# Performance work log

Hardware: AMD Instinct MI355X
Metric: run time of the kernel (lower is better)

Reference implementation:

```python
import jax, jax.numpy as jnp
import numpy as np

B, T, C = 4, 2048, 1024
N_HEADS = 16
HEAD_DIM = C // N_HEADS


def rotary_embedding(seq_len, dim, dtype=jnp.float32):
    pos = jnp.arange(seq_len, dtype=dtype)[:, None]
    i = jnp.arange(0, dim, 2, dtype=dtype)[None, :]
    theta = pos / jnp.power(10000.0, i / dim)
    return jnp.cos(theta), jnp.sin(theta)


def apply_rotary(x, cos, sin):
    # x: [B, T, H, D]; cos/sin: [T, D//2]
    d = x.shape[-1]
    x1, x2 = x[..., : d // 2], x[..., d // 2 :]
    rotated = jnp.concatenate([-x2, x1], axis=-1)
    cos = jnp.concatenate([cos, cos], axis=-1)[None, :, None, :]
    sin = jnp.concatenate([sin, sin], axis=-1)[None, :, None, :]
    return x * cos + rotated * sin


def setup_inputs() -> dict:
    key = jax.random.key(0)
    k1, k2, k3 = jax.random.split(key, 3)
    x = jax.random.normal(k1, (B, T, C), dtype=jnp.float32)
    # lecun_normal-ish init scale
    w_qkv = jax.random.normal(k2, (C, 3 * C), dtype=jnp.float32) / np.sqrt(C)
    w_out = jax.random.normal(k3, (C, C), dtype=jnp.float32) / np.sqrt(C)
    return {"x": x, "w_qkv": w_qkv, "w_out": w_out}


def reference(x, w_qkv, w_out):
    b, t, c = x.shape
    qkv = jnp.einsum("btc,cd->btd", x, w_qkv)
    q, k, v = jnp.split(qkv, 3, axis=-1)
    q = q.reshape(b, t, N_HEADS, HEAD_DIM)
    k = k.reshape(b, t, N_HEADS, HEAD_DIM)
    v = v.reshape(b, t, N_HEADS, HEAD_DIM)
    cos, sin = rotary_embedding(t, HEAD_DIM, dtype=x.dtype)
    q = apply_rotary(q, cos, sin)
    k = apply_rotary(k, cos, sin)
    scale = jnp.sqrt(jnp.asarray(HEAD_DIM, dtype=x.dtype))
    # scores: [B, H, T, T]
    attn = jnp.einsum("bqhd,bkhd->bhqk", q, k) / scale
    mask = jnp.tril(jnp.ones((t, t), dtype=jnp.bool_))
    attn = jnp.where(mask[None, None, :, :], attn, jnp.asarray(-1e9, dtype=x.dtype))
    attn = jax.nn.softmax(attn, axis=-1)
    out = jnp.einsum("bhqk,bkhd->bqhd", attn, v).reshape(b, t, c)
    return jnp.einsum("btc,cd->btd", out, w_out)
```

## Files before the change

kernel.cpp:

```cpp
#include <hip/hip_runtime.h>
#include <stdint.h>

#define DEVI __device__ __forceinline__

typedef unsigned short ushort_t;
typedef __bf16 bf16x8 __attribute__((ext_vector_type(8)));
typedef float f32x4 __attribute__((ext_vector_type(4)));
typedef unsigned short ushort8 __attribute__((ext_vector_type(8)));
typedef short s16x4 __attribute__((ext_vector_type(4)));

#define BB 4
#define TT 2048
#define CC 1024
#define NH 16
#define HD 64
#define MM (BB*TT)

DEVI ushort_t f2bf(float f) {
    union { float f; unsigned u; } v; v.f = f;
    return (ushort_t)((v.u + 0x7FFFu + ((v.u >> 16) & 1u)) >> 16);
}

typedef const __attribute__((address_space(1))) unsigned int guint_t;
typedef __attribute__((address_space(3))) unsigned int luint_t;

DEVI void gl2lds16(const void* g, void* lds) {
    __builtin_amdgcn_global_load_lds((guint_t*)(uintptr_t)g,
                                     (luint_t*)(unsigned int)(uintptr_t)lds,
                                     16, 0, 0);
}

__global__ void cvt_f32_bf16(const float* __restrict__ in,
                             ushort_t* __restrict__ out) {
    int i = blockIdx.x * 256 + threadIdx.x;
    const float4* p = (const float4*)in + (size_t)i * 2;
    float4 a = p[0], b = p[1];
    ushort8 r;
    r[0] = f2bf(a.x); r[1] = f2bf(a.y); r[2] = f2bf(a.z); r[3] = f2bf(a.w);
    r[4] = f2bf(b.x); r[5] = f2bf(b.y); r[6] = f2bf(b.z); r[7] = f2bf(b.w);
    *(ushort8*)(out + (size_t)i * 8) = r;
}

__global__ void transpose_f2b(const float* __restrict__ in,
                              ushort_t* __restrict__ out, int R, int Cc) {
    __shared__ ushort_t tile[32][33];
    int bx = blockIdx.x * 32;
    int by = blockIdx.y * 32;
    int tx = threadIdx.x & 31, ty = threadIdx.x >> 5;
    #pragma unroll
    for (int i = 0; i < 4; i++) {
        int r = ty * 4 + i;
        tile[r][tx] = f2bf(in[(size_t)(by + r) * Cc + bx + tx]);
    }
    __syncthreads();
    #pragma unroll
    for (int i = 0; i < 4; i++) {
        int r = ty * 4 + i;
        out[(size_t)(bx + r) * R + by + tx] = tile[tx][r];
    }
}

__global__ void rope_table(float2* __restrict__ tab) {
    int i = blockIdx.x * 256 + threadIdx.x;
    int t = i >> 5, j = i & 31;
    float inv = exp2f((float)j * -0.41524101186092029f);
    float theta = (float)t * inv;
    float s, c;
    sincosf(theta, &s, &c);
    tab[i] = make_float2(c, s);
}

__global__ void vtrans(const ushort_t* __restrict__ Vb,
                       ushort_t* __restrict__ VbT) {
    __shared__ ushort_t tile[64 * 72];
    const int bh = blockIdx.y;
    const int t0 = blockIdx.x * 64;
    const int tid = threadIdx.x;
    const int r = tid >> 2, c = (tid & 3) * 16;
    const size_t base = (size_t)bh * (TT * HD);
    const ushort_t* g = Vb + base + (size_t)(t0 + r) * HD + c;
    *(ushort8*)&tile[r * 72 + c]     = *(const ushort8*)g;
    *(ushort8*)&tile[r * 72 + c + 8] = *(const ushort8*)(g + 8);
    __syncthreads();
    ushort8 a, b;
    #pragma unroll
    for (int j = 0; j < 8; j++) a[j] = tile[(c + j) * 72 + r];
    #pragma unroll
    for (int j = 0; j < 8; j++) b[j] = tile[(c + 8 + j) * 72 + r];
    ushort_t* o = VbT + base + (size_t)r * TT + t0 + c;
    *(ushort8*)o = a;
    *(ushort8*)(o + 8) = b;
}

template <int MODE>
__global__ __launch_bounds__(256, 2) void gemm_bt(
    const ushort_t* __restrict__ A, const ushort_t* __restrict__ Bt,
    float* __restrict__ CoutF,
    ushort_t* __restrict__ Qb, ushort_t* __restrict__ Kb, ushort_t* __restrict__ Vb,
    const float2* __restrict__ rope, int M, int N, int Kd) {
    __shared__ __attribute__((aligned(16))) ushort_t As[128 * 32];
    __shared__ __attribute__((aligned(16))) ushort_t Bs[128 * 32];

    const int tid = threadIdx.x;
    const int w = tid >> 6, l = tid & 63;
    const int lane15 = l & 15, quad = l >> 4;
    const int wm = (w >> 1) * 64, wn = (w & 1) * 64;
    const int bm = blockIdx.y, bn = blockIdx.x;

    f32x4 acc[4][4];
    #pragma unroll
    for (int i = 0; i < 4; i++)
        #pragma unroll
        for (int j = 0; j < 4; j++)
            acc[i][j] = f32x4{0.f, 0.f, 0.f, 0.f};

    const int c0 = w * 2, c1 = w * 2 + 1;
    const int lr = l >> 2, lc = (l & 3) * 8;
    const int rowA0 = bm * 128 + c0 * 16 + lr;
    const int rowA1 = bm * 128 + c1 * 16 + lr;
    const ushort_t *gA0, *gA1;
    if (MODE == 2) {
        gA0 = A + ((size_t)(rowA0 >> 11) * 32768 + (rowA0 & (TT - 1))) * HD + lc;
        gA1 = A + ((size_t)(rowA1 >> 11) * 32768 + (rowA1 & (TT - 1))) * HD + lc;
    } else {
        gA0 = A + (size_t)rowA0 * Kd + lc;
        gA1 = A + (size_t)rowA1 * Kd + lc;
    }
    const ushort_t* gB0 = Bt + (size_t)(bn * 128 + c0 * 16 + lr) * Kd + lc;
    const ushort_t* gB1 = Bt + (size_t)(bn * 128 + c1 * 16 + lr) * Kd + lc;

    for (int k0 = 0; k0 < Kd; k0 += 32) {
        size_t offA = (MODE == 2) ? ((size_t)(k0 >> 6) * 131072 + (size_t)(k0 & 63))
                                  : (size_t)k0;
        __syncthreads();
        gl2lds16(gA0 + offA, &As[c0 * 512]);
        gl2lds16(gA1 + offA, &As[c1 * 512]);
        gl2lds16(gB0 + k0,  &Bs[c0 * 512]);
        gl2lds16(gB1 + k0,  &Bs[c1 * 512]);
        __syncthreads();

        bf16x8 af[4], bf[4];
        #pragma unroll
        for (int t = 0; t < 4; t++) {
            af[t] = *(const bf16x8*)&As[(wm + t * 16 + lane15) * 32 + quad * 8];
            bf[t] = *(const bf16x8*)&Bs[(wn + t * 16 + lane15) * 32 + quad * 8];
        }
        #pragma unroll
        for (int tm = 0; tm < 4; tm++)
            #pragma unroll
            for (int tn = 0; tn < 4; tn++)
                acc[tm][tn] = __builtin_amdgcn_mfma_f32_16x16x32_bf16(
                    af[tm], bf[tn], acc[tm][tn], 0, 0, 0);
    }

    if (MODE == 2) {
        #pragma unroll
        for (int tm = 0; tm < 4; tm++) {
            int row0 = bm * 128 + wm + tm * 16 + quad * 4;
            #pragma unroll
            for (int r = 0; r < 4; r++) {
                size_t rb = (size_t)(row0 + r) * N + bn * 128 + wn;
                #pragma unroll
                for (int tn = 0; tn < 4; tn++)
                    CoutF[rb + tn * 16 + lane15] = acc[tm][tn][r];
            }
        }
    } else {
        const float SCQ = 0.125f * 1.4426950408889634f;
        const int colbase = bn * 128 + wn;
        const int seg = colbase >> 10;
        const int h = (colbase & 1023) >> 6;
        #pragma unroll
        for (int tm = 0; tm < 4; tm++) {
            int row0 = bm * 128 + wm + tm * 16 + quad * 4;
            #pragma unroll
            for (int r = 0; r < 4; r++) {
                int row = row0 + r;
                int b = row >> 11, t = row & (TT - 1);
                size_t ob = ((size_t)(b * NH + h) * TT + t) * HD;
                if (seg == 2) {
                    #pragma unroll
                    for (int tn = 0; tn < 4; tn++)
                        Vb[ob + tn * 16 + lane15] = f2bf(acc[tm][tn][r]);
                } else {
                    ushort_t* dst = (seg == 0) ? Qb : Kb;
                    #pragma unroll
                    for (int tn = 0; tn < 2; tn++) {
                        int j = tn * 16 + lane15;
                        float2 cs = rope[t * 32 + j];
                        float x1 = acc[tm][tn][r];
                        float x2 = acc[tm][tn + 2][r];
                        float y1 = x1 * cs.x - x2 * cs.y;
                        float y2 = x2 * cs.x + x1 * cs.y;
                        if (seg == 0) { y1 *= SCQ; y2 *= SCQ; }
                        dst[ob + j]      = f2bf(y1);
                        dst[ob + 32 + j] = f2bf(y2);
                    }
                }
            }
        }
    }
}

__global__ __launch_bounds__(512, 4) void attn_kernel(
    ushort_t* __restrict__ Qb, const ushort_t* __restrict__ Kb,
    const ushort_t* __restrict__ VbT) {
    __shared__ __attribute__((aligned(16))) ushort_t Ks[64 * 72];
    __shared__ __attribute__((aligned(16))) ushort_t Vs[64 * 72];

    const int tid = threadIdx.x;
    const int w = tid >> 6, l = tid & 63;
    const int lane15 = l & 15, quad = l >> 4;
    const int bh = blockIdx.y;
    const size_t base = (size_t)bh * (TT * HD);

    const int sr = tid >> 3;
    const int sd = (tid & 7) * 8;
    const ushort_t* kgb = Kb  + base + (size_t)sr * HD + sd;
    const ushort_t* vgb = VbT + base + (size_t)sr * TT + sd;

    #pragma unroll
    for (int seg = 0; seg < 2; seg++) {
        const int qt = (seg == 0) ? (int)blockIdx.x : (15 - (int)blockIdx.x);
        const int q0 = qt * 128;
        const int rbase = q0 + w * 16;
        const int ktmax = 2 * qt + 1;

        bf16x8 qf0, qf1;
        {
            const ushort_t* qp = Qb + base + (size_t)(rbase + lane15) * HD + quad * 8;
            qf0 = *(const bf16x8*)qp;
            qf1 = *(const bf16x8*)(qp + 32);
        }

        f32x4 o[4];
        #pragma unroll
        for (int nt = 0; nt < 4; nt++) o[nt] = f32x4{0.f, 0.f, 0.f, 0.f};
        float mrow = -INFINITY, lrow = 0.f;

        ushort8 kr = *(const ushort8*)kgb;
        ushort8 vr = *(const ushort8*)vgb;

        for (int kt = 0; kt <= ktmax; kt++) {
            __syncthreads();
            *(ushort8*)&Ks[sr * 72 + sd] = kr;
            *(ushort8*)&Vs[sr * 72 + sd] = vr;
            __syncthreads();
            if (kt < ktmax) {
                kr = *(const ushort8*)(kgb + (size_t)(kt + 1) * 64 * HD);
                vr = *(const ushort8*)(vgb + (size_t)(kt + 1) * 64);
            }

            f32x4 s[4];
            #pragma unroll
            for (int c = 0; c < 4; c++) {
                bf16x8 k0 = *(const bf16x8*)&Ks[(c * 16 + lane15) * 72 + quad * 8];
                bf16x8 k1 = *(const bf16x8*)&Ks[(c * 16 + lane15) * 72 + 32 + quad * 8];
                f32x4 z = f32x4{0.f, 0.f, 0.f, 0.f};
                z = __builtin_amdgcn_mfma_f32_16x16x32_bf16(k0, qf0, z, 0, 0, 0);
                s[c] = __builtin_amdgcn_mfma_f32_16x16x32_bf16(k1, qf1, z, 0, 0, 0);
            }

            const int qrow = rbase + lane15;
            if (kt * 64 + 63 > rbase) {
                #pragma unroll
                for (int c = 0; c < 4; c++)
                    #pragma unroll
                    for (int r = 0; r < 4; r++)
                        if (kt * 64 + c * 16 + quad * 4 + r > qrow) s[c][r] = -1e9f;
            }

            float mt = s[0][0];
            #pragma unroll
            for (int c = 0; c < 4; c++)
                #pragma unroll
                for (int r = 0; r < 4; r++) mt = fmaxf(mt, s[c][r]);
            mt = fmaxf(mt, __shfl_xor(mt, 16, 64));
            mt = fmaxf(mt, __shfl_xor(mt, 32, 64));

            float mn = fmaxf(mrow, mt);
            float alpha = __builtin_amdgcn_exp2f(mrow - mn);
            mrow = mn;

            #pragma unroll
            for (int c = 0; c < 4; c++)
                #pragma unroll
                for (int r = 0; r < 4; r++)
                    s[c][r] = __builtin_amdgcn_exp2f(s[c][r] - mn);

            float rs = 0.f;
            #pragma unroll
            for (int c = 0; c < 4; c++)
                rs += (s[c][0] + s[c][1]) + (s[c][2] + s[c][3]);
            rs += __shfl_xor(rs, 16, 64);
            rs += __shfl_xor(rs, 32, 64);
            lrow = lrow * alpha + rs;

            #pragma unroll
            for (int r = 0; r < 4; r++) {
                float aO = __shfl(alpha, quad * 4 + r, 64);
                #pragma unroll
                for (int nt = 0; nt < 4; nt++) o[nt][r] *= aO;
            }

            #pragma unroll
            for (int c = 0; c < 4; c++) {
                s16x4 pf;
                #pragma unroll
                for (int r = 0; r < 4; r++) pf[r] = (short)f2bf(s[c][r]);
                #pragma unroll
                for (int nt = 0; nt < 4; nt++) {
                    s16x4 vf = *(const s16x4*)&Vs[(nt * 16 + lane15) * 72 +
                                                  c * 16 + quad * 4];
                    o[nt] = __builtin_amdgcn_mfma_f32_16x16x16bf16_1k(
                        pf, vf, o[nt], 0, 0, 0);
                }
            }
        }

        float linv = 1.0f / lrow;
        #pragma unroll
        for (int r = 0; r < 4; r++) {
            float lO = __shfl(linv, quad * 4 + r, 64);
            size_t rb = base + (size_t)(rbase + quad * 4 + r) * HD;
            #pragma unroll
            for (int nt = 0; nt < 4; nt++)
                Qb[rb + nt * 16 + lane15] = f2bf(o[nt][r] * lO);
        }
    }
}

extern "C" void kernel_launch(void* const* d_in, const int* in_sizes, int n_in,
                              void* d_out, int out_size, void* d_ws, size_t ws_size,
                              hipStream_t stream) {
    const float* x    = (const float*)d_in[0];
    const float* wqkv = (const float*)d_in[1];
    const float* wout = (const float*)d_in[2];
    float* out = (float*)d_out;

    char* ws = (char*)d_ws;
    ushort_t* WqkvT = (ushort_t*)(ws);
    ushort_t* WoutT = (ushort_t*)(ws + 6291456);
    float2*   rope  = (float2*)  (ws + 8388608);
    ushort_t* Xb    = (ushort_t*)(ws + 8912896);
    ushort_t* Qb    = (ushort_t*)(ws + 8912896 + 16777216);
    ushort_t* Kb    = (ushort_t*)(ws + 8912896 + 2 * 16777216);
    ushort_t* Vb    = (ushort_t*)(ws + 8912896 + 3 * 16777216);
    ushort_t* VbT   = Xb;

    cvt_f32_bf16<<<dim3(MM * CC / (256 * 8)), 256, 0, stream>>>(x, Xb);
    transpose_f2b<<<dim3(3 * CC / 32, CC / 32), 256, 0, stream>>>(wqkv, WqkvT, CC, 3 * CC);
    transpose_f2b<<<dim3(CC / 32, CC / 32), 256, 0, stream>>>(wout, WoutT, CC, CC);
    rope_table<<<dim3(256), 256, 0, stream>>>(rope);

    gemm_bt<1><<<dim3(3 * CC / 128, MM / 128), 256, 0, stream>>>(
        Xb, WqkvT, nullptr, Qb, Kb, Vb, rope, MM, 3 * CC, CC);

    vtrans<<<dim3(TT / 64, BB * NH), 256, 0, stream>>>(Vb, VbT);

    attn_kernel<<<dim3(8, BB * NH), 512, 0, stream>>>(Qb, Kb, VbT);

    gemm_bt<2><<<dim3(CC / 128, MM / 128), 256, 0, stream>>>(
        Qb, WoutT, out, nullptr, nullptr, nullptr, nullptr, MM, CC, CC);
}
```

Before: 279.3 us.

## Widen attention key tile to 128 and pack P to bf16 via perm truncation

```diff
diff --git a/kernel.cpp b/kernel.cpp
--- a/kernel.cpp
+++ b/kernel.cpp
@@ -8,6 +8,7 @@
 typedef float f32x4 __attribute__((ext_vector_type(4)));
 typedef unsigned short ushort8 __attribute__((ext_vector_type(8)));
 typedef short s16x4 __attribute__((ext_vector_type(4)));
+typedef unsigned int u32x2 __attribute__((ext_vector_type(2)));
 
 #define BB 4
 #define TT 2048
@@ -19,6 +20,11 @@
 DEVI ushort_t f2bf(float f) {
     union { float f; unsigned u; } v; v.f = f;
     return (ushort_t)((v.u + 0x7FFFu + ((v.u >> 16) & 1u)) >> 16);
+}
+
+DEVI unsigned pk_bf16(float lo, float hi) {
+    union { float f; unsigned u; } a, b; a.f = lo; b.f = hi;
+    return __builtin_amdgcn_perm(b.u, a.u, 0x07060302u);
 }
 
 typedef const __attribute__((address_space(1))) unsigned int guint_t;
@@ -202,29 +208,32 @@
     }
 }
 
+#define KS 72
+#define VS 136
 __global__ __launch_bounds__(512, 4) void attn_kernel(
     ushort_t* __restrict__ Qb, const ushort_t* __restrict__ Kb,
     const ushort_t* __restrict__ VbT) {
-    __shared__ __attribute__((aligned(16))) ushort_t Ks[64 * 72];
-    __shared__ __attribute__((aligned(16))) ushort_t Vs[64 * 72];
+    __shared__ __attribute__((aligned(16))) ushort_t Ks[128 * KS];
+    __shared__ __attribute__((aligned(16))) ushort_t Vs[64 * VS];
 
     const int tid = threadIdx.x;
-    const int w = tid >> 6, l = tid & 63;
+    const int l = tid & 63;
+    const int w = tid >> 6;
     const int lane15 = l & 15, quad = l >> 4;
     const int bh = blockIdx.y;
     const size_t base = (size_t)bh * (TT * HD);
 
-    const int sr = tid >> 3;
-    const int sd = (tid & 7) * 8;
-    const ushort_t* kgb = Kb  + base + (size_t)sr * HD + sd;
-    const ushort_t* vgb = VbT + base + (size_t)sr * TT + sd;
+    const int ksr = tid >> 3, ksd = (tid & 7) * 8;
+    const int vsr = tid >> 4, vsd = (tid & 15) * 8;
+    const ushort_t* kgb = Kb  + base + (size_t)ksr * HD + ksd;
+    const ushort_t* vgb = VbT + base + (size_t)vsr * TT + vsd;
 
     #pragma unroll
     for (int seg = 0; seg < 2; seg++) {
         const int qt = (seg == 0) ? (int)blockIdx.x : (15 - (int)blockIdx.x);
         const int q0 = qt * 128;
         const int rbase = q0 + w * 16;
-        const int ktmax = 2 * qt + 1;
+        const int ktmax = qt;
 
         bf16x8 qf0, qf1;
         {
@@ -238,43 +247,51 @@
         for (int nt = 0; nt < 4; nt++) o[nt] = f32x4{0.f, 0.f, 0.f, 0.f};
         float mrow = -INFINITY, lrow = 0.f;
 
-        ushort8 kr = *(const ushort8*)kgb;
-        ushort8 vr = *(const ushort8*)vgb;
+        ushort8 kr0 = *(const ushort8*)kgb;
+        ushort8 kr1 = *(const ushort8*)(kgb + (size_t)64 * HD);
+        ushort8 vr0 = *(const ushort8*)vgb;
+        ushort8 vr1 = *(const ushort8*)(vgb + (size_t)32 * TT);
 
         for (int kt = 0; kt <= ktmax; kt++) {
             __syncthreads();
-            *(ushort8*)&Ks[sr * 72 + sd] = kr;
-            *(ushort8*)&Vs[sr * 72 + sd] = vr;
+            *(ushort8*)&Ks[ksr * KS + ksd]        = kr0;
+            *(ushort8*)&Ks[(ksr + 64) * KS + ksd] = kr1;
+            *(ushort8*)&Vs[vsr * VS + vsd]        = vr0;
+            *(ushort8*)&Vs[(vsr + 32) * VS + vsd] = vr1;
             __syncthreads();
             if (kt < ktmax) {
-                kr = *(const ushort8*)(kgb + (size_t)(kt + 1) * 64 * HD);
-                vr = *(const ushort8*)(vgb + (size_t)(kt + 1) * 64);
-            }
-
-            f32x4 s[4];
-            #pragma unroll
-            for (int c = 0; c < 4; c++) {
-                bf16x8 k0 = *(const bf16x8*)&Ks[(c * 16 + lane15) * 72 + quad * 8];
-                bf16x8 k1 = *(const bf16x8*)&Ks[(c * 16 + lane15) * 72 + 32 + quad * 8];
+                const ushort_t* kg2 = kgb + (size_t)(kt + 1) * 128 * HD;
+                const ushort_t* vg2 = vgb + (size_t)(kt + 1) * 128;
+                kr0 = *(const ushort8*)kg2;
+                kr1 = *(const ushort8*)(kg2 + (size_t)64 * HD);
+                vr0 = *(const ushort8*)vg2;
+                vr1 = *(const ushort8*)(vg2 + (size_t)32 * TT);
+            }
+
+            f32x4 s[8];
+            #pragma unroll
+            for (int c = 0; c < 8; c++) {
+                bf16x8 k0 = *(const bf16x8*)&Ks[(c * 16 + lane15) * KS + quad * 8];
+                bf16x8 k1 = *(const bf16x8*)&Ks[(c * 16 + lane15) * KS + 32 + quad * 8];
                 f32x4 z = f32x4{0.f, 0.f, 0.f, 0.f};
                 z = __builtin_amdgcn_mfma_f32_16x16x32_bf16(k0, qf0, z, 0, 0, 0);
                 s[c] = __builtin_amdgcn_mfma_f32_16x16x32_bf16(k1, qf1, z, 0, 0, 0);
             }
 
             const int qrow = rbase + lane15;
-            if (kt * 64 + 63 > rbase) {
-                #pragma unroll
-                for (int c = 0; c < 4; c++)
+            if (kt == ktmax) {
+                #pragma unroll
+                for (int c = 0; c < 8; c++)
                     #pragma unroll
                     for (int r = 0; r < 4; r++)
-                        if (kt * 64 + c * 16 + quad * 4 + r > qrow) s[c][r] = -1e9f;
-            }
-
-            float mt = s[0][0];
-            #pragma unroll
-            for (int c = 0; c < 4; c++)
-                #pragma unroll
-                for (int r = 0; r < 4; r++) mt = fmaxf(mt, s[c][r]);
+                        if (kt * 128 + c * 16 + quad * 4 + r > qrow) s[c][r] = -1e9f;
+            }
+
+            float mt = fmaxf(fmaxf(fmaxf(s[0][0], s[0][1]), fmaxf(s[0][2], s[0][3])),
+                             fmaxf(fmaxf(s[1][0], s[1][1]), fmaxf(s[1][2], s[1][3])));
+            #pragma unroll
+            for (int c = 2; c < 8; c++)
+                mt = fmaxf(mt, fmaxf(fmaxf(s[c][0], s[c][1]), fmaxf(s[c][2], s[c][3])));
             mt = fmaxf(mt, __shfl_xor(mt, 16, 64));
             mt = fmaxf(mt, __shfl_xor(mt, 32, 64));
 
@@ -283,14 +300,14 @@
             mrow = mn;
 
             #pragma unroll
-            for (int c = 0; c < 4; c++)
+            for (int c = 0; c < 8; c++)
                 #pragma unroll
                 for (int r = 0; r < 4; r++)
                     s[c][r] = __builtin_amdgcn_exp2f(s[c][r] - mn);
 
             float rs = 0.f;
             #pragma unroll
-            for (int c = 0; c < 4; c++)
+            for (int c = 0; c < 8; c++)
                 rs += (s[c][0] + s[c][1]) + (s[c][2] + s[c][3]);
             rs += __shfl_xor(rs, 16, 64);
             rs += __shfl_xor(rs, 32, 64);
@@ -304,13 +321,14 @@
             }
 
             #pragma unroll
-            for (int c = 0; c < 4; c++) {
-                s16x4 pf;
-                #pragma unroll
-                for (int r = 0; r < 4; r++) pf[r] = (short)f2bf(s[c][r]);
+            for (int c = 0; c < 8; c++) {
+                u32x2 pd;
+                pd[0] = pk_bf16(s[c][0], s[c][1]);
+                pd[1] = pk_bf16(s[c][2], s[c][3]);
+                s16x4 pf = __builtin_bit_cast(s16x4, pd);
                 #pragma unroll
                 for (int nt = 0; nt < 4; nt++) {
-                    s16x4 vf = *(const s16x4*)&Vs[(nt * 16 + lane15) * 72 +
+                    s16x4 vf = *(const s16x4*)&Vs[(nt * 16 + lane15) * VS +
                                                   c * 16 + quad * 4];
                     o[nt] = __builtin_amdgcn_mfma_f32_16x16x16bf16_1k(
                         pf, vf, o[nt], 0, 0, 0);
```

Measured after the change: 288.8 us. +3.4%, slower.
